# Performance work log

Measured on AMD Instinct MI355X. Metric: run time of the kernel, lower is better.

Reference implementation:

```python
import jax, jax.numpy as jnp
import numpy as np

B = 1024          # batch
N = 2048          # number of gene groups
G = 32            # uniform group size (sum of gene_groups = N*G = 65536)
H1 = 2048         # hidden1_size
H2 = 512          # hidden2_size
EPS = 1e-5        # BatchNorm eps
SLOPE = 0.05      # LeakyReLU negative slope


def lrelu(v):
    return jnp.where(v >= 0, v, SLOPE * v)


def setup_inputs() -> dict:
    key = jax.random.key(0)
    ks = jax.random.split(key, 12)
    x = jax.random.normal(ks[0], (B, N * G), dtype=jnp.float32)
    # per-group Linear(G, 1) weights, stacked: [N, G] weights + [N] biases
    Wg = jax.random.normal(ks[1], (N, G), dtype=jnp.float32) / np.sqrt(G)
    bg = jax.random.normal(ks[2], (N,), dtype=jnp.float32) * 0.01
    att_w = jax.random.normal(ks[3], (N,), dtype=jnp.float32)
    W1 = jax.random.normal(ks[4], (N, H1), dtype=jnp.float32) / np.sqrt(N)
    b1 = jnp.zeros((H1,), dtype=jnp.float32)
    W2 = jax.random.normal(ks[5], (H1, H2), dtype=jnp.float32) / np.sqrt(H1)
    b2 = jnp.zeros((H2,), dtype=jnp.float32)
    Wo = jax.random.normal(ks[6], (H2, 1), dtype=jnp.float32) / np.sqrt(H2)
    bo = jnp.zeros((1,), dtype=jnp.float32)
    gamma1 = jnp.ones((H1,), dtype=jnp.float32)
    beta1 = jnp.zeros((H1,), dtype=jnp.float32)
    gamma2 = jnp.ones((H2,), dtype=jnp.float32)
    beta2 = jnp.zeros((H2,), dtype=jnp.float32)
    return dict(x=x, Wg=Wg, bg=bg, att_w=att_w, W1=W1, b1=b1,
                gamma1=gamma1, beta1=beta1, W2=W2, b2=b2,
                gamma2=gamma2, beta2=beta2, Wo=Wo, bo=bo)


def batchnorm(h, gamma, beta):
    # training-mode BatchNorm1d: batch statistics, biased variance
    mu = jnp.mean(h, axis=0)
    var = jnp.mean(jnp.square(h - mu), axis=0)
    return (h - mu) * jax.lax.rsqrt(var + EPS) * gamma + beta


def reference(x, Wg, bg, att_w, W1, b1, gamma1, beta1, W2, b2, gamma2, beta2, Wo, bo):
    # fused per-group linear + LeakyReLU: x viewed as [B, N, G]
    xg = x.reshape(B, N, G)
    g = lrelu(jnp.einsum('bng,ng->bn', xg, Wg) + bg)       # [B, N]
    att = jax.nn.softmax(att_w)                             # [N]
    a = g * att                                             # [B, N]
    h1 = lrelu(batchnorm(a @ W1 + b1, gamma1, beta1))       # [B, H1]
    h2 = lrelu(batchnorm(h1 @ W2 + b2, gamma2, beta2))      # [B, H2]
    return h2 @ Wo + bo                                     # [B, 1]
```

## Files before the change

### kernel.cpp

```cpp
#include <hip/hip_runtime.h>
#include <hip/hip_bf16.h>

#define B_DIM   1024
#define N_DIM   2048
#define G_DIM   32
#define H1_DIM  2048
#define H2_DIM  512
#define BN_EPS  1e-5f
#define SLOPE   0.05f

typedef short v8s __attribute__((ext_vector_type(8)));
typedef float v4f __attribute__((ext_vector_type(4)));

__device__ __forceinline__ float lrelu_f(float v) { return v >= 0.f ? v : SLOPE * v; }
__device__ __forceinline__ float bf2f(unsigned short u) {
    union { unsigned int i; float f; } c; c.i = ((unsigned int)u) << 16; return c.f;
}
__device__ __forceinline__ unsigned short f2bf(float f) {
    __hip_bfloat16 h = __float2bfloat16(f);
    return *(unsigned short*)&h;
}

#define GLOAD_LDS16(gp, lp)                                                              \
    __builtin_amdgcn_global_load_lds(                                                    \
        (const __attribute__((address_space(1))) unsigned int*)(gp),                     \
        (__attribute__((address_space(3))) unsigned int*)(lp), 16, 0, 0)

__global__ __launch_bounds__(256) void prep_kernel(
        const float* __restrict__ x, const float* __restrict__ Wg,
        const float* __restrict__ bg, __hip_bfloat16* __restrict__ g,
        const float* __restrict__ W1, const float* __restrict__ W2,
        const float* __restrict__ aw,
        __hip_bfloat16* __restrict__ W1T, __hip_bfloat16* __restrict__ W2T) {
    __shared__ float tile[64][65];
    __shared__ float red[8];
    __shared__ float scl[64];
    int t = threadIdx.x;
    int bid = blockIdx.x;

    if (bid < 2048) {
        int brow = bid >> 4;
        int seg = bid & 15;
        int gl = t >> 1, half = t & 1;
        int n = seg * 128 + gl;
        float4 wv[4];
        const float4* wsrc = (const float4*)(Wg + (size_t)n * 32 + half * 16);
#pragma unroll
        for (int q = 0; q < 4; ++q) wv[q] = wsrc[q];
        float bgv = bg[n];
#pragma unroll
        for (int bb = 0; bb < 8; ++bb) {
            int b = brow * 8 + bb;
            const float4* xr = (const float4*)(x + (size_t)b * (N_DIM * G_DIM) +
                                               (size_t)n * 32 + half * 16);
            float s = 0.f;
#pragma unroll
            for (int q = 0; q < 4; ++q) {
                float4 v = xr[q];
                s += v.x * wv[q].x + v.y * wv[q].y + v.z * wv[q].z + v.w * wv[q].w;
            }
            s += __shfl_xor(s, 1, 64);
            if (half == 0)
                g[(size_t)b * N_DIM + n] = __float2bfloat16(lrelu_f(s + bgv));
        }
        return;
    }

    const float* W;
    __hip_bfloat16* Wt;
    int Kd, Jd, j0, k0;
    bool doScale;
    int tb = bid - 2048;
    if (tb < 1024) {
        W = W1; Wt = W1T; Kd = N_DIM; Jd = H1_DIM;
        j0 = (tb & 31) * 64; k0 = (tb >> 5) * 64; doScale = true;
        float mx = -1e30f;
#pragma unroll
        for (int i = 0; i < 8; ++i) mx = fmaxf(mx, aw[t + i * 256]);
#pragma unroll
        for (int off = 32; off; off >>= 1) mx = fmaxf(mx, __shfl_xor(mx, off, 64));
        if ((t & 63) == 0) red[t >> 6] = mx;
        __syncthreads();
        float M = fmaxf(fmaxf(red[0], red[1]), fmaxf(red[2], red[3]));
        float sm = 0.f;
#pragma unroll
        for (int i = 0; i < 8; ++i) sm += expf(aw[t + i * 256] - M);
#pragma unroll
        for (int off = 32; off; off >>= 1) sm += __shfl_xor(sm, off, 64);
        if ((t & 63) == 0) red[4 + (t >> 6)] = sm;
        __syncthreads();
        float invS = 1.f / (red[4] + red[5] + red[6] + red[7]);
        if (t < 64) scl[t] = expf(aw[k0 + t] - M) * invS;
        __syncthreads();
    } else {
        int b2 = tb - 1024;
        W = W2; Wt = W2T; Kd = H1_DIM; Jd = H2_DIM;
        j0 = (b2 & 7) * 64; k0 = (b2 >> 3) * 64; doScale = false;
    }
#pragma unroll
    for (int p = 0; p < 16; ++p) {
        int r = (t >> 6) + p * 4;
        float v = W[(size_t)(k0 + r) * Jd + j0 + (t & 63)];
        if (doScale) v *= scl[r];
        tile[r][t & 63] = v;
    }
    __syncthreads();
#pragma unroll
    for (int p = 0; p < 8; ++p) {
        int jr = (t >> 5) + p * 8;
        int kc = (t & 31) * 2;
        ushort2 pk;
        pk.x = f2bf(tile[kc][jr]);
        pk.y = f2bf(tile[kc + 1][jr]);
        *(ushort2*)(Wt + (size_t)(j0 + jr) * Kd + k0 + kc) = pk;
    }
}

__global__ __launch_bounds__(256) void gemm1_stats(
        const __hip_bfloat16* __restrict__ A, const __hip_bfloat16* __restrict__ Bt,
        __hip_bfloat16* __restrict__ C, float* __restrict__ ps, float* __restrict__ pq) {
    __shared__ __hip_bfloat16 A_s[2][64 * 128];
    __shared__ __hip_bfloat16 B_s[2][64 * 128];
    __shared__ float rs[2][64], rq[2][64];

    int bid = blockIdx.x;
    int wg  = (bid & 7) * 64 + (bid >> 3);
    int bx  = wg & 15, by = wg >> 4;

    int tid = threadIdx.x, lane = tid & 63, wave = tid >> 6;
    int wr = wave >> 1, wc = wave & 1;
    int rbase = bx * 64, cbase = by * 64;
    int l15 = lane & 15, kq = lane >> 4;

    v4f acc[2][2] = {};

    auto stage = [&](int buf, int kt) {
        int k0 = kt << 7;
#pragma unroll
        for (int i = 0; i < 4; ++i) {
            int s = tid + i * 256;
            int row = s >> 4, cg = (s & 15) ^ (row & 15);
            GLOAD_LDS16(A + (size_t)(rbase + row) * N_DIM + k0 + cg * 8,
                        (char*)A_s[buf] + s * 16);
        }
#pragma unroll
        for (int i = 0; i < 4; ++i) {
            int s = tid + i * 256;
            int row = s >> 4, cg = (s & 15) ^ (row & 15);
            GLOAD_LDS16(Bt + (size_t)(cbase + row) * N_DIM + k0 + cg * 8,
                        (char*)B_s[buf] + s * 16);
        }
    };

    stage(0, 0);
    __syncthreads();
    int cur = 0;
    for (int kt = 0; kt < 16; ++kt) {
        if (kt + 1 < 16) stage(cur ^ 1, kt + 1);
#pragma unroll
        for (int kc = 0; kc < 4; ++kc) {
            v8s af[2], bfv[2];
#pragma unroll
            for (int m = 0; m < 2; ++m) {
                int row = wr * 32 + m * 16 + l15;
                int off = row * 256 + (((kc * 4 + kq) ^ (row & 15)) << 4);
                af[m] = *(const v8s*)((const char*)A_s[cur] + off);
            }
#pragma unroll
            for (int n = 0; n < 2; ++n) {
                int row = wc * 32 + n * 16 + l15;
                int off = row * 256 + (((kc * 4 + kq) ^ (row & 15)) << 4);
                bfv[n] = *(const v8s*)((const char*)B_s[cur] + off);
            }
            __builtin_amdgcn_s_setprio(1);
#pragma unroll
            for (int m = 0; m < 2; ++m)
#pragma unroll
                for (int n = 0; n < 2; ++n)
                    acc[m][n] = __builtin_amdgcn_mfma_f32_16x16x32_bf16(af[m], bfv[n],
                                                                        acc[m][n], 0, 0, 0);
            __builtin_amdgcn_s_setprio(0);
        }
        __syncthreads();
        cur ^= 1;
    }

    int crow = kq * 4;
#pragma unroll
    for (int m = 0; m < 2; ++m)
#pragma unroll
        for (int n = 0; n < 2; ++n) {
            int r = rbase + wr * 32 + m * 16 + crow;
            int c = cbase + wc * 32 + n * 16 + l15;
#pragma unroll
            for (int i = 0; i < 4; ++i)
                C[(size_t)(r + i) * H1_DIM + c] = __float2bfloat16(acc[m][n][i]);
        }

    float cs[2], cq[2];
#pragma unroll
    for (int n = 0; n < 2; ++n) {
        cs[n] = 0.f; cq[n] = 0.f;
#pragma unroll
        for (int m = 0; m < 2; ++m)
#pragma unroll
            for (int i = 0; i < 4; ++i) {
                float v = acc[m][n][i];
                cs[n] += v; cq[n] += v * v;
            }
#pragma unroll
        for (int off = 16; off <= 32; off <<= 1) {
            cs[n] += __shfl_xor(cs[n], off, 64);
            cq[n] += __shfl_xor(cq[n], off, 64);
        }
    }
    if (lane < 16) {
#pragma unroll
        for (int n = 0; n < 2; ++n) {
            rs[wr][wc * 32 + n * 16 + lane] = cs[n];
            rq[wr][wc * 32 + n * 16 + lane] = cq[n];
        }
    }
    __syncthreads();
    if (tid < 64) {
        ps[(size_t)bx * H1_DIM + cbase + tid] = rs[0][tid] + rs[1][tid];
        pq[(size_t)bx * H1_DIM + cbase + tid] = rq[0][tid] + rq[1][tid];
    }
}

__global__ __launch_bounds__(256) void gemm2_bn1(
        const __hip_bfloat16* __restrict__ h1pre, const __hip_bfloat16* __restrict__ W2T,
        float* __restrict__ h2raw,
        const float* __restrict__ ps1, const float* __restrict__ pq1,
        const float* __restrict__ gamma1, const float* __restrict__ beta1,
        float* __restrict__ ps2, float* __restrict__ pq2) {
    __shared__ float scl[H1_DIM], shf[H1_DIM];
    __shared__ __hip_bfloat16 A2[2][64 * 128];
    __shared__ __hip_bfloat16 B2[2][32 * 128];
    __shared__ float rs2[4][32], rq2[4][32];

    int tid = threadIdx.x, lane = tid & 63, wave = tid >> 6;
    int l15 = lane & 15, kq = lane >> 4;

#pragma unroll
    for (int p = 0; p < 8; ++p) {
        int c = tid + p * 256;
        float s = 0.f, q = 0.f;
#pragma unroll
        for (int i = 0; i < 16; ++i) {
            s += ps1[i * H1_DIM + c];
            q += pq1[i * H1_DIM + c];
        }
        float mu = s * (1.f / B_DIM);
        float var = fmaxf(q * (1.f / B_DIM) - mu * mu, 0.f);
        float rsv = rsqrtf(var + BN_EPS);
        float sc = rsv * gamma1[c];
        scl[c] = sc;
        shf[c] = beta1[c] - mu * sc;
    }
    __syncthreads();

    int bid = blockIdx.x;
    int wg = (bid & 7) * 32 + (bid >> 3);
    int bxx = wg & 15, byy = wg >> 4;
    int rb = bxx * 64, cb = byy * 32;

    v4f acc2[2] = {};

    auto stageA2 = [&](int buf, int kt) {
        int k0 = kt << 7;
#pragma unroll
        for (int i = 0; i < 4; ++i) {
            int s = tid + i * 256;
            int row = s >> 4, cc = s & 15;
            v8s hv = *(const v8s*)(h1pre + (size_t)(rb + row) * H1_DIM + k0 + cc * 8);
            int kk = k0 + cc * 8;
            float4 s0 = *(const float4*)&scl[kk];
            float4 s1 = *(const float4*)&scl[kk + 4];
            float4 f0 = *(const float4*)&shf[kk];
            float4 f1 = *(const float4*)&shf[kk + 4];
            v8s pk;
            pk[0] = (short)f2bf(lrelu_f(bf2f((unsigned short)hv[0]) * s0.x + f0.x));
            pk[1] = (short)f2bf(lrelu_f(bf2f((unsigned short)hv[1]) * s0.y + f0.y));
            pk[2] = (short)f2bf(lrelu_f(bf2f((unsigned short)hv[2]) * s0.z + f0.z));
            pk[3] = (short)f2bf(lrelu_f(bf2f((unsigned short)hv[3]) * s0.w + f0.w));
            pk[4] = (short)f2bf(lrelu_f(bf2f((unsigned short)hv[4]) * s1.x + f1.x));
            pk[5] = (short)f2bf(lrelu_f(bf2f((unsigned short)hv[5]) * s1.y + f1.y));
            pk[6] = (short)f2bf(lrelu_f(bf2f((unsigned short)hv[6]) * s1.z + f1.z));
            pk[7] = (short)f2bf(lrelu_f(bf2f((unsigned short)hv[7]) * s1.w + f1.w));
            *(v8s*)((char*)A2[buf] + (row * 16 + (cc ^ (row & 15))) * 16) = pk;
        }
    };
    auto stageB2 = [&](int buf, int kt) {
        int k0 = kt << 7;
#pragma unroll
        for (int i = 0; i < 2; ++i) {
            int s = tid + i * 256;
            int row = s >> 4, cg2 = (s & 15) ^ (row & 15);
            GLOAD_LDS16(W2T + (size_t)(cb + row) * H1_DIM + k0 + cg2 * 8,
                        (char*)B2[buf] + s * 16);
        }
    };

    stageB2(0, 0);
    stageA2(0, 0);
    __syncthreads();
    int cur = 0;
    for (int kt = 0; kt < 16; ++kt) {
        if (kt + 1 < 16) { stageB2(cur ^ 1, kt + 1); stageA2(cur ^ 1, kt + 1); }
#pragma unroll
        for (int kc = 0; kc < 4; ++kc) {
            int arow = wave * 16 + l15;
            v8s af = *(const v8s*)((const char*)A2[cur] +
                                   arow * 256 + (((kc * 4 + kq) ^ (arow & 15)) << 4));
            v8s bf0 = *(const v8s*)((const char*)B2[cur] +
                                    l15 * 256 + (((kc * 4 + kq) ^ (l15 & 15)) << 4));
            int brow1 = 16 + l15;
            v8s bf1 = *(const v8s*)((const char*)B2[cur] +
                                    brow1 * 256 + (((kc * 4 + kq) ^ (brow1 & 15)) << 4));
            __builtin_amdgcn_s_setprio(1);
            acc2[0] = __builtin_amdgcn_mfma_f32_16x16x32_bf16(af, bf0, acc2[0], 0, 0, 0);
            acc2[1] = __builtin_amdgcn_mfma_f32_16x16x32_bf16(af, bf1, acc2[1], 0, 0, 0);
            __builtin_amdgcn_s_setprio(0);
        }
        __syncthreads();
        cur ^= 1;
    }

    int crow = kq * 4;
#pragma unroll
    for (int n = 0; n < 2; ++n) {
        int r = rb + wave * 16 + crow;
        int c = cb + n * 16 + l15;
#pragma unroll
        for (int i = 0; i < 4; ++i)
            h2raw[(size_t)(r + i) * H2_DIM + c] = acc2[n][i];
    }

    float cs[2], cq[2];
#pragma unroll
    for (int n = 0; n < 2; ++n) {
        cs[n] = 0.f; cq[n] = 0.f;
#pragma unroll
        for (int i = 0; i < 4; ++i) {
            float v = acc2[n][i];
            cs[n] += v; cq[n] += v * v;
        }
#pragma unroll
        for (int off = 16; off <= 32; off <<= 1) {
            cs[n] += __shfl_xor(cs[n], off, 64);
            cq[n] += __shfl_xor(cq[n], off, 64);
        }
    }
    if (lane < 16) {
#pragma unroll
        for (int n = 0; n < 2; ++n) {
            rs2[wave][n * 16 + lane] = cs[n];
            rq2[wave][n * 16 + lane] = cq[n];
        }
    }
    __syncthreads();
    if (tid < 32) {
        float s = 0.f, q = 0.f;
#pragma unroll
        for (int w = 0; w < 4; ++w) { s += rs2[w][tid]; q += rq2[w][tid]; }
        ps2[(size_t)bxx * H2_DIM + cb + tid] = s;
        pq2[(size_t)bxx * H2_DIM + cb + tid] = q;
    }
}

__global__ __launch_bounds__(256) void bn_dot_fused(
        const float* __restrict__ h2,
        const float* __restrict__ ps, const float* __restrict__ pq,
        const float* __restrict__ gamma, const float* __restrict__ beta,
        const float* __restrict__ Wo, const float* __restrict__ bo,
        float* __restrict__ out) {
    __shared__ float scl[H2_DIM], shf[H2_DIM];
    __shared__ float red[4][4];
    int t = threadIdx.x;
#pragma unroll
    for (int p = 0; p < 2; ++p) {
        int c = t + p * 256;
        float s = 0.f, q = 0.f;
#pragma unroll
        for (int i = 0; i < 16; ++i) {
            s += ps[i * H2_DIM + c];
            q += pq[i * H2_DIM + c];
        }
        float mu = s * (1.f / B_DIM);
        float var = fmaxf(q * (1.f / B_DIM) - mu * mu, 0.f);
        float rsv = rsqrtf(var + BN_EPS);
        float sc = rsv * gamma[c];
        scl[c] = sc;
        shf[c] = beta[c] - mu * sc;
    }
    __syncthreads();
    float accv[4];
#pragma unroll
    for (int r = 0; r < 4; ++r) {
        int b = blockIdx.x * 4 + r;
        float s = 0.f;
#pragma unroll
        for (int p = 0; p < 2; ++p) {
            int jj = t + p * 256;
            float v = lrelu_f(h2[(size_t)b * H2_DIM + jj] * scl[jj] + shf[jj]);
            s += v * Wo[jj];
        }
#pragma unroll
        for (int off = 32; off; off >>= 1) s += __shfl_down(s, off, 64);
        accv[r] = s;
    }
    if ((t & 63) == 0) {
#pragma unroll
        for (int r = 0; r < 4; ++r) red[t >> 6][r] = accv[r];
    }
    __syncthreads();
    if (t < 4)
        out[blockIdx.x * 4 + t] = red[0][t] + red[1][t] + red[2][t] + red[3][t] + bo[0];
}

extern "C" void kernel_launch(void* const* d_in, const int* in_sizes, int n_in,
                              void* d_out, int out_size, void* d_ws, size_t ws_size,
                              hipStream_t stream) {
    const float* x     = (const float*)d_in[0];
    const float* Wg    = (const float*)d_in[1];
    const float* bg    = (const float*)d_in[2];
    const float* att_w = (const float*)d_in[3];
    const float* W1    = (const float*)d_in[4];
    const float* gamma1 = (const float*)d_in[6];
    const float* beta1  = (const float*)d_in[7];
    const float* W2    = (const float*)d_in[8];
    const float* gamma2 = (const float*)d_in[10];
    const float* beta2  = (const float*)d_in[11];
    const float* Wo    = (const float*)d_in[12];
    const float* bo    = (const float*)d_in[13];
    float* out = (float*)d_out;

    char* ws = (char*)d_ws;
    size_t off = 0;
    auto alloc = [&](size_t bytes) {
        void* p = ws + off;
        off = (off + bytes + 255) & ~(size_t)255;
        return p;
    };
    __hip_bfloat16* W1T   = (__hip_bfloat16*)alloc((size_t)H1_DIM * N_DIM * 2);
    __hip_bfloat16* W2T   = (__hip_bfloat16*)alloc((size_t)H2_DIM * H1_DIM * 2);
    __hip_bfloat16* g     = (__hip_bfloat16*)alloc((size_t)B_DIM * N_DIM * 2);
    __hip_bfloat16* h1pre = (__hip_bfloat16*)alloc((size_t)B_DIM * H1_DIM * 2);
    float*          h2raw = (float*)alloc((size_t)B_DIM * H2_DIM * 4);
    float*          ps1   = (float*)alloc(16 * H1_DIM * 4);
    float*          pq1   = (float*)alloc(16 * H1_DIM * 4);
    float*          ps2   = (float*)alloc(16 * H2_DIM * 4);
    float*          pq2   = (float*)alloc(16 * H2_DIM * 4);
    (void)ws_size; (void)in_sizes; (void)n_in; (void)out_size;

    prep_kernel<<<dim3(2048 + 1024 + 256), 256, 0, stream>>>(x, Wg, bg, g,
                                                             W1, W2, att_w, W1T, W2T);
    gemm1_stats<<<dim3(512), 256, 0, stream>>>(g, W1T, h1pre, ps1, pq1);
    gemm2_bn1<<<dim3(256), 256, 0, stream>>>(h1pre, W2T, h2raw, ps1, pq1,
                                             gamma1, beta1, ps2, pq2);
    bn_dot_fused<<<dim3(B_DIM / 4), 256, 0, stream>>>(h2raw, ps2, pq2, gamma2, beta2,
                                                      Wo, bo, out);
}
```

Before: 104.3 us.

## Fuse GEMM1, GEMM2 and final BN-dot into one persistent kernel with grid barriers

Merges the three post-prep kernels into a single 512-block kernel that uses atomic-counter grid barriers between the GEMM1+stats, GEMM2+BN1 and BN2+dot phases. Shared memory is reused across phases through one byte buffer. This removes two kernel launch gaps and tail idle time but needs all 512 blocks co-resident (launch bounds set to 2 blocks per CU), adds a memset, and leaves half the blocks idle during the GEMM2 phase.

```diff
diff --git a/kernel.cpp b/kernel.cpp
--- a/kernel.cpp
+++ b/kernel.cpp
@@ -25,6 +25,18 @@
     __builtin_amdgcn_global_load_lds(                                                    \
         (const __attribute__((address_space(1))) unsigned int*)(gp),                     \
         (__attribute__((address_space(3))) unsigned int*)(lp), 16, 0, 0)
+
+__device__ __forceinline__ void grid_barrier(unsigned int* cnt, unsigned int nblk, int tid) {
+    __threadfence();
+    __syncthreads();
+    if (tid == 0) {
+        __hip_atomic_fetch_add(cnt, 1u, __ATOMIC_ACQ_REL, __HIP_MEMORY_SCOPE_AGENT);
+        while (__hip_atomic_load(cnt, __ATOMIC_ACQUIRE, __HIP_MEMORY_SCOPE_AGENT) < nblk)
+            __builtin_amdgcn_s_sleep(2);
+    }
+    __syncthreads();
+    __threadfence();
+}
 
 __global__ __launch_bounds__(256) void prep_kernel(
         const float* __restrict__ x, const float* __restrict__ Wg,
@@ -116,307 +128,305 @@
     }
 }
 
-__global__ __launch_bounds__(256) void gemm1_stats(
-        const __hip_bfloat16* __restrict__ A, const __hip_bfloat16* __restrict__ Bt,
-        __hip_bfloat16* __restrict__ C, float* __restrict__ ps, float* __restrict__ pq) {
-    __shared__ __hip_bfloat16 A_s[2][64 * 128];
-    __shared__ __hip_bfloat16 B_s[2][64 * 128];
-    __shared__ float rs[2][64], rq[2][64];
-
+__global__ __launch_bounds__(256, 2) void fused_main(
+        const __hip_bfloat16* __restrict__ g, const __hip_bfloat16* __restrict__ W1T,
+        const __hip_bfloat16* __restrict__ W2T,
+        __hip_bfloat16* __restrict__ h1pre, float* __restrict__ h2raw,
+        float* __restrict__ ps1, float* __restrict__ pq1,
+        float* __restrict__ ps2, float* __restrict__ pq2,
+        const float* __restrict__ gamma1, const float* __restrict__ beta1,
+        const float* __restrict__ gamma2, const float* __restrict__ beta2,
+        const float* __restrict__ Wo, const float* __restrict__ bo,
+        float* __restrict__ out, unsigned int* __restrict__ cnts) {
+    __shared__ __align__(16) char smem[66560];
+    int tid = threadIdx.x, lane = tid & 63, wave = tid >> 6;
     int bid = blockIdx.x;
-    int wg  = (bid & 7) * 64 + (bid >> 3);
-    int bx  = wg & 15, by = wg >> 4;
-
-    int tid = threadIdx.x, lane = tid & 63, wave = tid >> 6;
-    int wr = wave >> 1, wc = wave & 1;
-    int rbase = bx * 64, cbase = by * 64;
     int l15 = lane & 15, kq = lane >> 4;
 
-    v4f acc[2][2] = {};
-
-    auto stage = [&](int buf, int kt) {
-        int k0 = kt << 7;
-#pragma unroll
-        for (int i = 0; i < 4; ++i) {
-            int s = tid + i * 256;
-            int row = s >> 4, cg = (s & 15) ^ (row & 15);
-            GLOAD_LDS16(A + (size_t)(rbase + row) * N_DIM + k0 + cg * 8,
-                        (char*)A_s[buf] + s * 16);
-        }
-#pragma unroll
-        for (int i = 0; i < 4; ++i) {
-            int s = tid + i * 256;
-            int row = s >> 4, cg = (s & 15) ^ (row & 15);
-            GLOAD_LDS16(Bt + (size_t)(cbase + row) * N_DIM + k0 + cg * 8,
-                        (char*)B_s[buf] + s * 16);
-        }
-    };
-
-    stage(0, 0);
-    __syncthreads();
-    int cur = 0;
-    for (int kt = 0; kt < 16; ++kt) {
-        if (kt + 1 < 16) stage(cur ^ 1, kt + 1);
-#pragma unroll
-        for (int kc = 0; kc < 4; ++kc) {
-            v8s af[2], bfv[2];
-#pragma unroll
-            for (int m = 0; m < 2; ++m) {
-                int row = wr * 32 + m * 16 + l15;
-                int off = row * 256 + (((kc * 4 + kq) ^ (row & 15)) << 4);
-                af[m] = *(const v8s*)((const char*)A_s[cur] + off);
-            }
+    {
+        __hip_bfloat16 (*A_s)[64 * 128] = (__hip_bfloat16(*)[64 * 128])(smem);
+        __hip_bfloat16 (*B_s)[64 * 128] = (__hip_bfloat16(*)[64 * 128])(smem + 32768);
+        float* rs1 = (float*)(smem + 65536);
+        float* rq1 = (float*)(smem + 66048);
+
+        int wg = (bid & 7) * 64 + (bid >> 3);
+        int bx = wg & 15, by = wg >> 4;
+        int wr = wave >> 1, wc = wave & 1;
+        int rbase = bx * 64, cbase = by * 64;
+
+        v4f acc[2][2] = {};
+
+        auto stage = [&](int buf, int kt) {
+            int k0 = kt << 7;
+#pragma unroll
+            for (int i = 0; i < 4; ++i) {
+                int s = tid + i * 256;
+                int row = s >> 4, cg2 = (s & 15) ^ (row & 15);
+                GLOAD_LDS16(g + (size_t)(rbase + row) * N_DIM + k0 + cg2 * 8,
+                            (char*)A_s[buf] + s * 16);
+            }
+#pragma unroll
+            for (int i = 0; i < 4; ++i) {
+                int s = tid + i * 256;
+                int row = s >> 4, cg2 = (s & 15) ^ (row & 15);
+                GLOAD_LDS16(W1T + (size_t)(cbase + row) * N_DIM + k0 + cg2 * 8,
+                            (char*)B_s[buf] + s * 16);
+            }
+        };
+
+        stage(0, 0);
+        __syncthreads();
+        int cur = 0;
+        for (int kt = 0; kt < 16; ++kt) {
+            if (kt + 1 < 16) stage(cur ^ 1, kt + 1);
+#pragma unroll
+            for (int kc = 0; kc < 4; ++kc) {
+                v8s af[2], bfv[2];
+#pragma unroll
+                for (int m = 0; m < 2; ++m) {
+                    int row = wr * 32 + m * 16 + l15;
+                    int off = row * 256 + (((kc * 4 + kq) ^ (row & 15)) << 4);
+                    af[m] = *(const v8s*)((const char*)A_s[cur] + off);
+                }
+#pragma unroll
+                for (int n = 0; n < 2; ++n) {
+                    int row = wc * 32 + n * 16 + l15;
+                    int off = row * 256 + (((kc * 4 + kq) ^ (row & 15)) << 4);
+                    bfv[n] = *(const v8s*)((const char*)B_s[cur] + off);
+                }
+                __builtin_amdgcn_s_setprio(1);
+#pragma unroll
+                for (int m = 0; m < 2; ++m)
+#pragma unroll
+                    for (int n = 0; n < 2; ++n)
+                        acc[m][n] = __builtin_amdgcn_mfma_f32_16x16x32_bf16(af[m], bfv[n],
+                                                                            acc[m][n], 0, 0, 0);
+                __builtin_amdgcn_s_setprio(0);
+            }
+            __syncthreads();
+            cur ^= 1;
+        }
+
+        int crow = kq * 4;
+#pragma unroll
+        for (int m = 0; m < 2; ++m)
 #pragma unroll
             for (int n = 0; n < 2; ++n) {
-                int row = wc * 32 + n * 16 + l15;
-                int off = row * 256 + (((kc * 4 + kq) ^ (row & 15)) << 4);
-                bfv[n] = *(const v8s*)((const char*)B_s[cur] + off);
-            }
-            __builtin_amdgcn_s_setprio(1);
+                int r = rbase + wr * 32 + m * 16 + crow;
+                int c = cbase + wc * 32 + n * 16 + l15;
+#pragma unroll
+                for (int i = 0; i < 4; ++i)
+                    h1pre[(size_t)(r + i) * H1_DIM + c] = __float2bfloat16(acc[m][n][i]);
+            }
+
+        float cs[2], cq[2];
+#pragma unroll
+        for (int n = 0; n < 2; ++n) {
+            cs[n] = 0.f; cq[n] = 0.f;
 #pragma unroll
             for (int m = 0; m < 2; ++m)
 #pragma unroll
-                for (int n = 0; n < 2; ++n)
-                    acc[m][n] = __builtin_amdgcn_mfma_f32_16x16x32_bf16(af[m], bfv[n],
-                                                                        acc[m][n], 0, 0, 0);
-            __builtin_amdgcn_s_setprio(0);
-        }
-        __syncthreads();
-        cur ^= 1;
-    }
-
-    int crow = kq * 4;
-#pragma unroll
-    for (int m = 0; m < 2; ++m)
+                for (int i = 0; i < 4; ++i) {
+                    float v = acc[m][n][i];
+                    cs[n] += v; cq[n] += v * v;
+                }
+#pragma unroll
+            for (int off = 16; off <= 32; off <<= 1) {
+                cs[n] += __shfl_xor(cs[n], off, 64);
+                cq[n] += __shfl_xor(cq[n], off, 64);
+            }
+        }
+        if (lane < 16) {
+#pragma unroll
+            for (int n = 0; n < 2; ++n) {
+                rs1[wr * 64 + wc * 32 + n * 16 + lane] = cs[n];
+                rq1[wr * 64 + wc * 32 + n * 16 + lane] = cq[n];
+            }
+        }
+        __syncthreads();
+        if (tid < 64) {
+            ps1[(size_t)bx * H1_DIM + cbase + tid] = rs1[tid] + rs1[64 + tid];
+            pq1[(size_t)bx * H1_DIM + cbase + tid] = rq1[tid] + rq1[64 + tid];
+        }
+    }
+
+    grid_barrier(&cnts[0], 512u, tid);
+
+    if (bid < 256) {
+        float* scl = (float*)(smem);
+        float* shf = (float*)(smem + 8192);
+        __hip_bfloat16 (*A2)[64 * 128] = (__hip_bfloat16(*)[64 * 128])(smem + 16384);
+        __hip_bfloat16 (*B2)[32 * 128] = (__hip_bfloat16(*)[32 * 128])(smem + 49152);
+        float* rs2 = (float*)(smem + 65536);
+        float* rq2 = (float*)(smem + 66048);
+
+#pragma unroll
+        for (int p = 0; p < 8; ++p) {
+            int c = tid + p * 256;
+            float s = 0.f, q = 0.f;
+#pragma unroll
+            for (int i = 0; i < 16; ++i) {
+                s += ps1[i * H1_DIM + c];
+                q += pq1[i * H1_DIM + c];
+            }
+            float mu = s * (1.f / B_DIM);
+            float var = fmaxf(q * (1.f / B_DIM) - mu * mu, 0.f);
+            float rsv = rsqrtf(var + BN_EPS);
+            float sc = rsv * gamma1[c];
+            scl[c] = sc;
+            shf[c] = beta1[c] - mu * sc;
+        }
+        __syncthreads();
+
+        int wg = (bid & 7) * 32 + (bid >> 3);
+        int bxx = wg & 15, byy = wg >> 4;
+        int rb = bxx * 64, cb = byy * 32;
+
+        v4f acc2[2] = {};
+
+        auto stageA2 = [&](int buf, int kt) {
+            int k0 = kt << 7;
+#pragma unroll
+            for (int i = 0; i < 4; ++i) {
+                int s = tid + i * 256;
+                int row = s >> 4, cc = s & 15;
+                v8s hv = *(const v8s*)(h1pre + (size_t)(rb + row) * H1_DIM + k0 + cc * 8);
+                int kk = k0 + cc * 8;
+                float4 s0 = *(const float4*)&scl[kk];
+                float4 s1 = *(const float4*)&scl[kk + 4];
+                float4 f0 = *(const float4*)&shf[kk];
+                float4 f1 = *(const float4*)&shf[kk + 4];
+                v8s pk;
+                pk[0] = (short)f2bf(lrelu_f(bf2f((unsigned short)hv[0]) * s0.x + f0.x));
+                pk[1] = (short)f2bf(lrelu_f(bf2f((unsigned short)hv[1]) * s0.y + f0.y));
+                pk[2] = (short)f2bf(lrelu_f(bf2f((unsigned short)hv[2]) * s0.z + f0.z));
+                pk[3] = (short)f2bf(lrelu_f(bf2f((unsigned short)hv[3]) * s0.w + f0.w));
+                pk[4] = (short)f2bf(lrelu_f(bf2f((unsigned short)hv[4]) * s1.x + f1.x));
+                pk[5] = (short)f2bf(lrelu_f(bf2f((unsigned short)hv[5]) * s1.y + f1.y));
+                pk[6] = (short)f2bf(lrelu_f(bf2f((unsigned short)hv[6]) * s1.z + f1.z));
+                pk[7] = (short)f2bf(lrelu_f(bf2f((unsigned short)hv[7]) * s1.w + f1.w));
+                *(v8s*)((char*)A2[buf] + (row * 16 + (cc ^ (row & 15))) * 16) = pk;
+            }
+        };
+        auto stageB2 = [&](int buf, int kt) {
+            int k0 = kt << 7;
+#pragma unroll
+            for (int i = 0; i < 2; ++i) {
+                int s = tid + i * 256;
+                int row = s >> 4, cg2 = (s & 15) ^ (row & 15);
+                GLOAD_LDS16(W2T + (size_t)(cb + row) * H1_DIM + k0 + cg2 * 8,
+                            (char*)B2[buf] + s * 16);
+            }
+        };
+
+        stageB2(0, 0);
+        stageA2(0, 0);
+        __syncthreads();
+        int cur = 0;
+        for (int kt = 0; kt < 16; ++kt) {
+            if (kt + 1 < 16) { stageB2(cur ^ 1, kt + 1); stageA2(cur ^ 1, kt + 1); }
+#pragma unroll
+            for (int kc = 0; kc < 4; ++kc) {
+                int arow = wave * 16 + l15;
+                v8s af = *(const v8s*)((const char*)A2[cur] +
+                                       arow * 256 + (((kc * 4 + kq) ^ (arow & 15)) << 4));
+                v8s bf0 = *(const v8s*)((const char*)B2[cur] +
+                                        l15 * 256 + (((kc * 4 + kq) ^ (l15 & 15)) << 4));
+                int brow1 = 16 + l15;
+                v8s bf1 = *(const v8s*)((const char*)B2[cur] +
+                                        brow1 * 256 + (((kc * 4 + kq) ^ (brow1 & 15)) << 4));
+                __builtin_amdgcn_s_setprio(1);
+                acc2[0] = __builtin_amdgcn_mfma_f32_16x16x32_bf16(af, bf0, acc2[0], 0, 0, 0);
+                acc2[1] = __builtin_amdgcn_mfma_f32_16x16x32_bf16(af, bf1, acc2[1], 0, 0, 0);
+                __builtin_amdgcn_s_setprio(0);
+            }
+            __syncthreads();
+            cur ^= 1;
+        }
+
+        int crow = kq * 4;
 #pragma unroll
         for (int n = 0; n < 2; ++n) {
-            int r = rbase + wr * 32 + m * 16 + crow;
-            int c = cbase + wc * 32 + n * 16 + l15;
+            int r = rb + wave * 16 + crow;
+            int c = cb + n * 16 + l15;
 #pragma unroll
             for (int i = 0; i < 4; ++i)
-                C[(size_t)(r + i) * H1_DIM + c] = __float2bfloat16(acc[m][n][i]);
-        }
-
-    float cs[2], cq[2];
-#pragma unroll
-    for (int n = 0; n < 2; ++n) {
-        cs[n] = 0.f; cq[n] = 0.f;
-#pragma unroll
-        for (int m = 0; m < 2; ++m)
+                h2raw[(size_t)(r + i) * H2_DIM + c] = acc2[n][i];
+        }
+
+        float cs[2], cq[2];
+#pragma unroll
+        for (int n = 0; n < 2; ++n) {
+            cs[n] = 0.f; cq[n] = 0.f;
 #pragma unroll
             for (int i = 0; i < 4; ++i) {
-                float v = acc[m][n][i];
+                float v = acc2[n][i];
                 cs[n] += v; cq[n] += v * v;
             }
 #pragma unroll
-        for (int off = 16; off <= 32; off <<= 1) {
-            cs[n] += __shfl_xor(cs[n], off, 64);
-            cq[n] += __shfl_xor(cq[n], off, 64);
-        }
-    }
-    if (lane < 16) {
-#pragma unroll
-        for (int n = 0; n < 2; ++n) {
-            rs[wr][wc * 32 + n * 16 + lane] = cs[n];
-            rq[wr][wc * 32 + n * 16 + lane] = cq[n];
-        }
-    }
-    __syncthreads();
-    if (tid < 64) {
-        ps[(size_t)bx * H1_DIM + cbase + tid] = rs[0][tid] + rs[1][tid];
-        pq[(size_t)bx * H1_DIM + cbase + tid] = rq[0][tid] + rq[1][tid];
-    }
-}
-
-__global__ __launch_bounds__(256) void gemm2_bn1(
-        const __hip_bfloat16* __restrict__ h1pre, const __hip_bfloat16* __restrict__ W2T,
-        float* __restrict__ h2raw,
-        const float* __restrict__ ps1, const float* __restrict__ pq1,
-        const float* __restrict__ gamma1, const float* __restrict__ beta1,
-        float* __restrict__ ps2, float* __restrict__ pq2) {
-    __shared__ float scl[H1_DIM], shf[H1_DIM];
-    __shared__ __hip_bfloat16 A2[2][64 * 128];
-    __shared__ __hip_bfloat16 B2[2][32 * 128];
-    __shared__ float rs2[4][32], rq2[4][32];
-
-    int tid = threadIdx.x, lane = tid & 63, wave = tid >> 6;
-    int l15 = lane & 15, kq = lane >> 4;
-
-#pragma unroll
-    for (int p = 0; p < 8; ++p) {
-        int c = tid + p * 256;
-        float s = 0.f, q = 0.f;
-#pragma unroll
-        for (int i = 0; i < 16; ++i) {
-            s += ps1[i * H1_DIM + c];
-            q += pq1[i * H1_DIM + c];
-        }
-        float mu = s * (1.f / B_DIM);
-        float var = fmaxf(q * (1.f / B_DIM) - mu * mu, 0.f);
-        float rsv = rsqrtf(var + BN_EPS);
-        float sc = rsv * gamma1[c];
-        scl[c] = sc;
-        shf[c] = beta1[c] - mu * sc;
-    }
-    __syncthreads();
-
-    int bid = blockIdx.x;
-    int wg = (bid & 7) * 32 + (bid >> 3);
-    int bxx = wg & 15, byy = wg >> 4;
-    int rb = bxx * 64, cb = byy * 32;
-
-    v4f acc2[2] = {};
-
-    auto stageA2 = [&](int buf, int kt) {
-        int k0 = kt << 7;
-#pragma unroll
-        for (int i = 0; i < 4; ++i) {
-            int s = tid + i * 256;
-            int row = s >> 4, cc = s & 15;
-            v8s hv = *(const v8s*)(h1pre + (size_t)(rb + row) * H1_DIM + k0 + cc * 8);
-            int kk = k0 + cc * 8;
-            float4 s0 = *(const float4*)&scl[kk];
-            float4 s1 = *(const float4*)&scl[kk + 4];
-            float4 f0 = *(const float4*)&shf[kk];
-            float4 f1 = *(const float4*)&shf[kk + 4];
-            v8s pk;
-            pk[0] = (short)f2bf(lrelu_f(bf2f((unsigned short)hv[0]) * s0.x + f0.x));
-            pk[1] = (short)f2bf(lrelu_f(bf2f((unsigned short)hv[1]) * s0.y + f0.y));
-            pk[2] = (short)f2bf(lrelu_f(bf2f((unsigned short)hv[2]) * s0.z + f0.z));
-            pk[3] = (short)f2bf(lrelu_f(bf2f((unsigned short)hv[3]) * s0.w + f0.w));
-            pk[4] = (short)f2bf(lrelu_f(bf2f((unsigned short)hv[4]) * s1.x + f1.x));
-            pk[5] = (short)f2bf(lrelu_f(bf2f((unsigned short)hv[5]) * s1.y + f1.y));
-            pk[6] = (short)f2bf(lrelu_f(bf2f((unsigned short)hv[6]) * s1.z + f1.z));
-            pk[7] = (short)f2bf(lrelu_f(bf2f((unsigned short)hv[7]) * s1.w + f1.w));
-            *(v8s*)((char*)A2[buf] + (row * 16 + (cc ^ (row & 15))) * 16) = pk;
-        }
-    };
-    auto stageB2 = [&](int buf, int kt) {
-        int k0 = kt << 7;
-#pragma unroll
-        for (int i = 0; i < 2; ++i) {
-            int s = tid + i * 256;
-            int row = s >> 4, cg2 = (s & 15) ^ (row & 15);
-            GLOAD_LDS16(W2T + (size_t)(cb + row) * H1_DIM + k0 + cg2 * 8,
-                        (char*)B2[buf] + s * 16);
-        }
-    };
-
-    stageB2(0, 0);
-    stageA2(0, 0);
-    __syncthreads();
-    int cur = 0;
-    for (int kt = 0; kt < 16; ++kt) {
-        if (kt + 1 < 16) { stageB2(cur ^ 1, kt + 1); stageA2(cur ^ 1, kt + 1); }
-#pragma unroll
-        for (int kc = 0; kc < 4; ++kc) {
-            int arow = wave * 16 + l15;
-            v8s af = *(const v8s*)((const char*)A2[cur] +
-                                   arow * 256 + (((kc * 4 + kq) ^ (arow & 15)) << 4));
-            v8s bf0 = *(const v8s*)((const char*)B2[cur] +
-                                    l15 * 256 + (((kc * 4 + kq) ^ (l15 & 15)) << 4));
-            int brow1 = 16 + l15;
-            v8s bf1 = *(const v8s*)((const char*)B2[cur] +
-                                    brow1 * 256 + (((kc * 4 + kq) ^ (brow1 & 15)) << 4));
-            __builtin_amdgcn_s_setprio(1);
-            acc2[0] = __builtin_amdgcn_mfma_f32_16x16x32_bf16(af, bf0, acc2[0], 0, 0, 0);
-            acc2[1] = __builtin_amdgcn_mfma_f32_16x16x32_bf16(af, bf1, acc2[1], 0, 0, 0);
-            __builtin_amdgcn_s_setprio(0);
-        }
-        __syncthreads();
-        cur ^= 1;
-    }
-
-    int crow = kq * 4;
-#pragma unroll
-    for (int n = 0; n < 2; ++n) {
-        int r = rb + wave * 16 + crow;
-        int c = cb + n * 16 + l15;
-#pragma unroll
-        for (int i = 0; i < 4; ++i)
-            h2raw[(size_t)(r + i) * H2_DIM + c] = acc2[n][i];
-    }
-
-    float cs[2], cq[2];
-#pragma unroll
-    for (int n = 0; n < 2; ++n) {
-        cs[n] = 0.f; cq[n] = 0.f;
-#pragma unroll
-        for (int i = 0; i < 4; ++i) {
-            float v = acc2[n][i];
-            cs[n] += v; cq[n] += v * v;
-        }
-#pragma unroll
-        for (int off = 16; off <= 32; off <<= 1) {
-            cs[n] += __shfl_xor(cs[n], off, 64);
-            cq[n] += __shfl_xor(cq[n], off, 64);
-        }
-    }
-    if (lane < 16) {
-#pragma unroll
-        for (int n = 0; n < 2; ++n) {
-            rs2[wave][n * 16 + lane] = cs[n];
-            rq2[wave][n * 16 + lane] = cq[n];
-        }
-    }
-    __syncthreads();
-    if (tid < 32) {
-        float s = 0.f, q = 0.f;
-#pragma unroll
-        for (int w = 0; w < 4; ++w) { s += rs2[w][tid]; q += rq2[w][tid]; }
-        ps2[(size_t)bxx * H2_DIM + cb + tid] = s;
-        pq2[(size_t)bxx * H2_DIM + cb + tid] = q;
-    }
-}
-
-__global__ __launch_bounds__(256) void bn_dot_fused(
-        const float* __restrict__ h2,
-        const float* __restrict__ ps, const float* __restrict__ pq,
-        const float* __restrict__ gamma, const float* __restrict__ beta,
-        const float* __restrict__ Wo, const float* __restrict__ bo,
-        float* __restrict__ out) {
-    __shared__ float scl[H2_DIM], shf[H2_DIM];
-    __shared__ float red[4][4];
-    int t = threadIdx.x;
-#pragma unroll
-    for (int p = 0; p < 2; ++p) {
-        int c = t + p * 256;
-        float s = 0.f, q = 0.f;
-#pragma unroll
-        for (int i = 0; i < 16; ++i) {
-            s += ps[i * H2_DIM + c];
-            q += pq[i * H2_DIM + c];
-        }
-        float mu = s * (1.f / B_DIM);
-        float var = fmaxf(q * (1.f / B_DIM) - mu * mu, 0.f);
-        float rsv = rsqrtf(var + BN_EPS);
-        float sc = rsv * gamma[c];
-        scl[c] = sc;
-        shf[c] = beta[c] - mu * sc;
-    }
-    __syncthreads();
-    float accv[4];
-#pragma unroll
-    for (int r = 0; r < 4; ++r) {
-        int b = blockIdx.x * 4 + r;
-        float s = 0.f;
+            for (int off = 16; off <= 32; off <<= 1) {
+                cs[n] += __shfl_xor(cs[n], off, 64);
+                cq[n] += __shfl_xor(cq[n], off, 64);
+            }
+        }
+        if (lane < 16) {
+#pragma unroll
+            for (int n = 0; n < 2; ++n) {
+                rs2[wave * 32 + n * 16 + lane] = cs[n];
+                rq2[wave * 32 + n * 16 + lane] = cq[n];
+            }
+        }
+        __syncthreads();
+        if (tid < 32) {
+            float s = 0.f, q = 0.f;
+#pragma unroll
+            for (int w = 0; w < 4; ++w) { s += rs2[w * 32 + tid]; q += rq2[w * 32 + tid]; }
+            ps2[(size_t)bxx * H2_DIM + cb + tid] = s;
+            pq2[(size_t)bxx * H2_DIM + cb + tid] = q;
+        }
+    }
+
+    grid_barrier(&cnts[1], 512u, tid);
+
+    {
+        float* scl2 = (float*)(smem);
+        float* shf2 = (float*)(smem + 2048);
+        float* red  = (float*)(smem + 4096);
 #pragma unroll
         for (int p = 0; p < 2; ++p) {
-            int jj = t + p * 256;
-            float v = lrelu_f(h2[(size_t)b * H2_DIM + jj] * scl[jj] + shf[jj]);
-            s += v * Wo[jj];
-        }
-#pragma unroll
-        for (int off = 32; off; off >>= 1) s += __shfl_down(s, off, 64);
-        accv[r] = s;
-    }
-    if ((t & 63) == 0) {
-#pragma unroll
-        for (int r = 0; r < 4; ++r) red[t >> 6][r] = accv[r];
-    }
-    __syncthreads();
-    if (t < 4)
-        out[blockIdx.x * 4 + t] = red[0][t] + red[1][t] + red[2][t] + red[3][t] + bo[0];
+            int c = tid + p * 256;
+            float s = 0.f, q = 0.f;
+#pragma unroll
+            for (int i = 0; i < 16; ++i) {
+                s += ps2[i * H2_DIM + c];
+                q += pq2[i * H2_DIM + c];
+            }
+            float mu = s * (1.f / B_DIM);
+            float var = fmaxf(q * (1.f / B_DIM) - mu * mu, 0.f);
+            float rsv = rsqrtf(var + BN_EPS);
+            float sc = rsv * gamma2[c];
+            scl2[c] = sc;
+            shf2[c] = beta2[c] - mu * sc;
+        }
+        __syncthreads();
+#pragma unroll
+        for (int rr = 0; rr < 2; ++rr) {
+            int b = bid * 2 + rr;
+            float s = 0.f;
+#pragma unroll
+            for (int p = 0; p < 2; ++p) {
+                int j = tid + p * 256;
+                float v = lrelu_f(h2raw[(size_t)b * H2_DIM + j] * scl2[j] + shf2[j]);
+                s += v * Wo[j];
+            }
+#pragma unroll
+            for (int off = 32; off; off >>= 1) s += __shfl_down(s, off, 64);
+            if (lane == 0) red[wave] = s;
+            __syncthreads();
+            if (tid == 0) out[b] = red[0] + red[1] + red[2] + red[3] + bo[0];
+            __syncthreads();
+        }
+    }
 }
 
 extern "C" void kernel_launch(void* const* d_in, const int* in_sizes, int n_in,
@@ -452,13 +462,14 @@
     float*          pq1   = (float*)alloc(16 * H1_DIM * 4);
     float*          ps2   = (float*)alloc(16 * H2_DIM * 4);
     float*          pq2   = (float*)alloc(16 * H2_DIM * 4);
+    unsigned int*   cnts  = (unsigned int*)alloc(256);
     (void)ws_size; (void)in_sizes; (void)n_in; (void)out_size;
 
+    hipMemsetAsync(cnts, 0, 8, stream);
     prep_kernel<<<dim3(2048 + 1024 + 256), 256, 0, stream>>>(x, Wg, bg, g,
                                                              W1, W2, att_w, W1T, W2T);
-    gemm1_stats<<<dim3(512), 256, 0, stream>>>(g, W1T, h1pre, ps1, pq1);
-    gemm2_bn1<<<dim3(256), 256, 0, stream>>>(h1pre, W2T, h2raw, ps1, pq1,
-                                             gamma1, beta1, ps2, pq2);
-    bn_dot_fused<<<dim3(B_DIM / 4), 256, 0, stream>>>(h2raw, ps2, pq2, gamma2, beta2,
-                                                      Wo, bo, out);
-}
+    fused_main<<<dim3(512), 256, 0, stream>>>(g, W1T, W2T, h1pre, h2raw,
+                                              ps1, pq1, ps2, pq2,
+                                              gamma1, beta1, gamma2, beta2,
+                                              Wo, bo, out, cnts);
+}
```

Result: slower. 378.9 us (+263.4%).
